# Performance work log

Hardware: AMD Instinct MI355X
Metric: run time of the kernel (lower is better)

The kernel has to match this reference:

```python
import jax, jax.numpy as jnp
import numpy as np

VOCAB, EMBED, MAXLEN, UNITS, F1, BATCH = 50000, 256, 512, 32, 16, 512

def setup_inputs() -> dict:
    key = jax.random.key(0)
    ks = jax.random.split(key, 9)
    tokens = jax.random.randint(ks[0], (BATCH, MAXLEN), 0, VOCAB, dtype=jnp.int32)
    emb_table = jax.random.normal(ks[1], (VOCAB, EMBED), dtype=jnp.float32) * 0.02
    # SimpleRNN params (Keras: kernel, recurrent_kernel, bias)
    Wx = jax.random.normal(ks[2], (EMBED, UNITS), dtype=jnp.float32) * (1.0 / np.sqrt(EMBED))
    Wh = jax.random.normal(ks[3], (UNITS, UNITS), dtype=jnp.float32) * (1.0 / np.sqrt(UNITS))
    b  = jnp.zeros((UNITS,), dtype=jnp.float32)
    W1 = jax.random.normal(ks[4], (UNITS, F1), dtype=jnp.float32) * (1.0 / np.sqrt(UNITS))
    b1 = jnp.zeros((F1,), dtype=jnp.float32)
    W2 = jax.random.normal(ks[5], (F1, 1), dtype=jnp.float32) * (1.0 / np.sqrt(F1))
    b2 = jnp.zeros((1,), dtype=jnp.float32)
    return {"tokens": tokens, "emb_table": emb_table, "Wx": Wx, "Wh": Wh, "b": b,
            "W1": W1, "b1": b1, "W2": W2, "b2": b2}

def reference(tokens, emb_table, Wx, Wh, b, W1, b1, W2, b2):
    # Embedding lookup: [B, T, E]
    x = emb_table[tokens]
    # SimpleRNN recurrence (tanh), return last hidden state. Dropout disabled (inference).
    xs = jnp.transpose(x, (1, 0, 2))  # time-major [T, B, E]
    h0 = jnp.zeros((tokens.shape[0], Wh.shape[0]), dtype=x.dtype)

    def step(h, x_t):
        h_new = jnp.tanh(x_t @ Wx + h @ Wh + b)
        return h_new, None

    h_last, _ = jax.lax.scan(step, h0, xs)
    # Flatten is a no-op on [B, 32]; Dense heads are linear (no activation), then sigmoid.
    z = (h_last @ W1 + b1) @ W2 + b2
    return jax.nn.sigmoid(z)  # [B, 1]
```

## Files before the change

kernel.cpp:

```cpp
#include <hip/hip_runtime.h>
#include <hip/hip_bf16.h>
#include <math.h>

#define TT 512
#define BB 512
#define EE 256
#define UU 32
#define FF1 16
#define NWAVE 2048

#define TWO_LOG2E 2.8853900817779268f

__device__ __forceinline__ float rdlane(float v, int lane) {
    return __int_as_float(__builtin_amdgcn_readlane(__float_as_int(v), lane));
}

#define DPP_ADD(v, ctrl)                                                    \
    (v) += __int_as_float(__builtin_amdgcn_update_dpp(                      \
        0, __float_as_int(v), (ctrl), 0xf, 0xf, true))

__global__ __launch_bounds__(64) void proj_dpp(
    const float* __restrict__ emb, const float* __restrict__ Wx,
    const float* __restrict__ bias, float* __restrict__ P, int nrows)
{
    const int L = threadIdx.x;
    const int g = L >> 4;
    const int c = L & 15;
    const int wv = blockIdx.x;

    float w[16][8];
    #pragma unroll
    for (int kk = 0; kk < 16; ++kk) {
        const float4* src = (const float4*)(Wx + (size_t)(kk * 16 + c) * UU + g * 8);
        float4 a = src[0], b = src[1];
        w[kk][0] = a.x; w[kk][1] = a.y; w[kk][2] = a.z; w[kk][3] = a.w;
        w[kk][4] = b.x; w[kk][5] = b.y; w[kk][6] = b.z; w[kk][7] = b.w;
    }
    float bs[8];
    #pragma unroll
    for (int uu = 0; uu < 8; ++uu) bs[uu] = bias[g * 8 + uu];

    auto rowptr = [&](int i) {
        int r = wv + NWAVE * i;
        if (r >= nrows) r = nrows - 1;
        return emb + (size_t)r * EE;
    };

    float xA[16], xB[16];
    {
        const float* rp = rowptr(0);
        #pragma unroll
        for (int kk = 0; kk < 16; ++kk) xA[kk] = rp[kk * 16 + c];
    }

    const int NI = (nrows - 1 - wv) / NWAVE + 1;

    for (int i = 0; i < NI; ++i) {
        {
            const float* rp = rowptr(i + 1 < NI ? i + 1 : i);
            #pragma unroll
            for (int kk = 0; kk < 16; ++kk) xB[kk] = rp[kk * 16 + c];
        }

        float p[8];
        #pragma unroll
        for (int uu = 0; uu < 8; ++uu) p[uu] = 0.f;
        #pragma unroll
        for (int kk = 0; kk < 16; ++kk) {
            const float xk = xA[kk];
            #pragma unroll
            for (int uu = 0; uu < 8; ++uu)
                p[uu] = fmaf(xk, w[kk][uu], p[uu]);
        }

        #pragma unroll
        for (int uu = 0; uu < 8; ++uu) {
            DPP_ADD(p[uu], 0x111);
            DPP_ADD(p[uu], 0x112);
            DPP_ADD(p[uu], 0x114);
            DPP_ADD(p[uu], 0x118);
        }

        if (c == 15) {
            const int r = wv + NWAVE * i;
            float4 o0, o1;
            o0.x = (p[0] + bs[0]) * TWO_LOG2E;
            o0.y = (p[1] + bs[1]) * TWO_LOG2E;
            o0.z = (p[2] + bs[2]) * TWO_LOG2E;
            o0.w = (p[3] + bs[3]) * TWO_LOG2E;
            o1.x = (p[4] + bs[4]) * TWO_LOG2E;
            o1.y = (p[5] + bs[5]) * TWO_LOG2E;
            o1.z = (p[6] + bs[6]) * TWO_LOG2E;
            o1.w = (p[7] + bs[7]) * TWO_LOG2E;
            float4* dst = (float4*)(P + (size_t)r * UU + g * 8);
            dst[0] = o0; dst[1] = o1;
        }

        #pragma unroll
        for (int kk = 0; kk < 16; ++kk) xA[kk] = xB[kk];
    }
}

__global__ __launch_bounds__(64) void scan_heads(
    const int* __restrict__ tokens, const float* __restrict__ P,
    const float* __restrict__ Wh,
    const float* __restrict__ W1, const float* __restrict__ b1,
    const float* __restrict__ W2, const float* __restrict__ b2,
    float* __restrict__ out)
{
    __shared__ float xs[TT * UU];

    const int L = threadIdx.x;
    const int u = L & 31;
    const int b = blockIdx.x;
    const int* trow = tokens + b * TT;

    float wh[UU];
    #pragma unroll
    for (int k = 0; k < UU; ++k) wh[k] = Wh[k * UU + u] * TWO_LOG2E;

    const int sub = L >> 3;
    const int q   = L & 7;
    for (int c = 0; c < 8; ++c) {
        int tk8[8];
        #pragma unroll
        for (int i = 0; i < 8; ++i)
            tk8[i] = trow[c * 64 + i * 8 + sub];
        #pragma unroll
        for (int i = 0; i < 8; ++i) {
            const float* src = P + (size_t)tk8[i] * UU + q * 4;
            float* dst = xs + (c * 64 + i * 8) * UU;
            __builtin_amdgcn_global_load_lds(
                (const __attribute__((address_space(1))) void*)src,
                (__attribute__((address_space(3))) void*)dst, 16, 0, 0);
        }
    }
    __syncthreads();

    float xr[8];
    #pragma unroll
    for (int j = 0; j < 8; ++j) xr[j] = xs[j * UU + u];

    float h = 0.f;

    for (int t = 0; t < TT; t += 8) {
        float xn[8];
        #pragma unroll
        for (int j = 0; j < 8; ++j)
            xn[j] = xs[((t + 8 + j) & (TT - 1)) * UU + u];

        #pragma unroll
        for (int j = 0; j < 8; ++j) {
            float hv[UU];
            #pragma unroll
            for (int k = 0; k < UU; ++k) hv[k] = rdlane(h, k);

            float a0 = fmaf(hv[0], wh[0], xr[j]);
            float a1 = hv[1] * wh[1];
            float a2 = hv[2] * wh[2];
            float a3 = hv[3] * wh[3];
            #pragma unroll
            for (int k = 4; k < UU; k += 4) {
                a0 = fmaf(hv[k],     wh[k],     a0);
                a1 = fmaf(hv[k + 1], wh[k + 1], a1);
                a2 = fmaf(hv[k + 2], wh[k + 2], a2);
                a3 = fmaf(hv[k + 3], wh[k + 3], a3);
            }
            float e = __builtin_amdgcn_exp2f((a0 + a1) + (a2 + a3));
            float r = __builtin_amdgcn_rcpf(e + 1.0f);
            h = fmaf(-2.0f, r, 1.0f);
        }

        #pragma unroll
        for (int j = 0; j < 8; ++j) xr[j] = xn[j];
    }

    const int j = threadIdx.x & 15;
    float s = b1[j];
    #pragma unroll
    for (int k = 0; k < UU; ++k) {
        float hk = rdlane(h, k);
        s = fmaf(hk, W1[k * FF1 + j], s);
    }
    float z = b2[0];
    #pragma unroll
    for (int jj = 0; jj < FF1; ++jj) {
        float yj = rdlane(s, jj);
        z = fmaf(yj, W2[jj], z);
    }
    if (threadIdx.x == 0) {
        float e = __builtin_amdgcn_exp2f(-z * 1.4426950408889634f);
        out[b] = __builtin_amdgcn_rcpf(1.0f + e);
    }
}

extern "C" void kernel_launch(void* const* d_in, const int* in_sizes, int n_in,
                              void* d_out, int out_size, void* d_ws, size_t ws_size,
                              hipStream_t stream) {
    const int*   tokens = (const int*)  d_in[0];
    const float* emb    = (const float*)d_in[1];
    const float* Wx     = (const float*)d_in[2];
    const float* Wh     = (const float*)d_in[3];
    const float* bias   = (const float*)d_in[4];
    const float* W1     = (const float*)d_in[5];
    const float* b1     = (const float*)d_in[6];
    const float* W2     = (const float*)d_in[7];
    const float* b2     = (const float*)d_in[8];
    float* out = (float*)d_out;

    const int vocab = in_sizes[1] / EE;
    float* P = (float*)d_ws;

    proj_dpp<<<dim3(NWAVE), dim3(64), 0, stream>>>(
        emb, Wx, bias, P, vocab);

    scan_heads<<<dim3(BB), dim3(64), 0, stream>>>(
        tokens, P, Wh, W1, b1, W2, b2, out);
}
```

Baseline: 182.7 us.

## Carry sigmoid-domain state in RNN scan and vectorize projection loads

The scan now carries r = 1/(1+e) as its state instead of h, folding h = 1 - 2r into the weights (wr = -2*wh) and into a per-unit constant S added to the inputs. This removes the final fma from the serial dependency chain of each step. Only the first 32 lanes run the scan, and the loop is double-buffered over 16 steps. Separately, the projection kernel loads embedding rows as float2 with a matching weight reorder, halving its load instructions; the algebraic refactor may change rounding slightly.

Measured after the change: 189.9 us. 3.9% more time.

```diff
diff --git a/kernel.cpp b/kernel.cpp
--- a/kernel.cpp
+++ b/kernel.cpp
@@ -28,49 +28,56 @@
     const int c = L & 15;
     const int wv = blockIdx.x;
 
-    float w[16][8];
+    float w[8][2][8];
     #pragma unroll
-    for (int kk = 0; kk < 16; ++kk) {
-        const float4* src = (const float4*)(Wx + (size_t)(kk * 16 + c) * UU + g * 8);
-        float4 a = src[0], b = src[1];
-        w[kk][0] = a.x; w[kk][1] = a.y; w[kk][2] = a.z; w[kk][3] = a.w;
-        w[kk][4] = b.x; w[kk][5] = b.y; w[kk][6] = b.z; w[kk][7] = b.w;
+    for (int kk = 0; kk < 8; ++kk) {
+        #pragma unroll
+        for (int d = 0; d < 2; ++d) {
+            const int row = 32 * kk + 2 * c + d;
+            const float4* src = (const float4*)(Wx + (size_t)row * UU + g * 8);
+            float4 a = src[0], b = src[1];
+            w[kk][d][0] = a.x; w[kk][d][1] = a.y; w[kk][d][2] = a.z; w[kk][d][3] = a.w;
+            w[kk][d][4] = b.x; w[kk][d][5] = b.y; w[kk][d][6] = b.z; w[kk][d][7] = b.w;
+        }
     }
     float bs[8];
     #pragma unroll
     for (int uu = 0; uu < 8; ++uu) bs[uu] = bias[g * 8 + uu];
 
-    auto rowptr = [&](int i) {
+    auto rowptr2 = [&](int i) {
         int r = wv + NWAVE * i;
         if (r >= nrows) r = nrows - 1;
-        return emb + (size_t)r * EE;
+        return (const float2*)(emb + (size_t)r * EE);
     };
 
-    float xA[16], xB[16];
+    float2 xA[8], xB[8];
     {
-        const float* rp = rowptr(0);
-        #pragma unroll
-        for (int kk = 0; kk < 16; ++kk) xA[kk] = rp[kk * 16 + c];
+        const float2* rp = rowptr2(0);
+        #pragma unroll
+        for (int kk = 0; kk < 8; ++kk) xA[kk] = rp[kk * 16 + c];
     }
 
     const int NI = (nrows - 1 - wv) / NWAVE + 1;
 
     for (int i = 0; i < NI; ++i) {
         {
-            const float* rp = rowptr(i + 1 < NI ? i + 1 : i);
-            #pragma unroll
-            for (int kk = 0; kk < 16; ++kk) xB[kk] = rp[kk * 16 + c];
+            const float2* rp = rowptr2(i + 1 < NI ? i + 1 : i);
+            #pragma unroll
+            for (int kk = 0; kk < 8; ++kk) xB[kk] = rp[kk * 16 + c];
         }
 
         float p[8];
         #pragma unroll
         for (int uu = 0; uu < 8; ++uu) p[uu] = 0.f;
         #pragma unroll
-        for (int kk = 0; kk < 16; ++kk) {
-            const float xk = xA[kk];
+        for (int kk = 0; kk < 8; ++kk) {
+            const float2 xp = xA[kk];
             #pragma unroll
             for (int uu = 0; uu < 8; ++uu)
-                p[uu] = fmaf(xk, w[kk][uu], p[uu]);
+                p[uu] = fmaf(xp.x, w[kk][0][uu], p[uu]);
+            #pragma unroll
+            for (int uu = 0; uu < 8; ++uu)
+                p[uu] = fmaf(xp.y, w[kk][1][uu], p[uu]);
         }
 
         #pragma unroll
@@ -97,7 +104,7 @@
         }
 
         #pragma unroll
-        for (int kk = 0; kk < 16; ++kk) xA[kk] = xB[kk];
+        for (int kk = 0; kk < 8; ++kk) xA[kk] = xB[kk];
     }
 }
 
@@ -115,9 +122,14 @@
     const int b = blockIdx.x;
     const int* trow = tokens + b * TT;
 
-    float wh[UU];
+    float wr[UU];
+    float S = 0.f;
     #pragma unroll
-    for (int k = 0; k < UU; ++k) wh[k] = Wh[k * UU + u] * TWO_LOG2E;
+    for (int k = 0; k < UU; ++k) {
+        float whk = Wh[k * UU + u] * TWO_LOG2E;
+        S += whk;
+        wr[k] = -2.0f * whk;
+    }
 
     const int sub = L >> 3;
     const int q   = L & 7;
@@ -137,60 +149,65 @@
     }
     __syncthreads();
 
-    float xr[8];
-    #pragma unroll
-    for (int j = 0; j < 8; ++j) xr[j] = xs[j * UU + u];
-
-    float h = 0.f;
-
-    for (int t = 0; t < TT; t += 8) {
-        float xn[8];
-        #pragma unroll
-        for (int j = 0; j < 8; ++j)
-            xn[j] = xs[((t + 8 + j) & (TT - 1)) * UU + u];
-
-        #pragma unroll
-        for (int j = 0; j < 8; ++j) {
-            float hv[UU];
-            #pragma unroll
-            for (int k = 0; k < UU; ++k) hv[k] = rdlane(h, k);
-
-            float a0 = fmaf(hv[0], wh[0], xr[j]);
-            float a1 = hv[1] * wh[1];
-            float a2 = hv[2] * wh[2];
-            float a3 = hv[3] * wh[3];
+    if (L < 32) {
+        float xA[8], xB[8];
+        #pragma unroll
+        for (int j = 0; j < 8; ++j) xA[j] = xs[j * UU + u] + S;
+
+        float r = 0.5f;
+
+        auto step = [&](float rc, float x) -> float {
+            float rv[UU];
+            #pragma unroll
+            for (int k = 0; k < UU; ++k) rv[k] = rdlane(rc, k);
+
+            float a0 = fmaf(rv[0], wr[0], x);
+            float a1 = rv[1] * wr[1];
+            float a2 = rv[2] * wr[2];
+            float a3 = rv[3] * wr[3];
             #pragma unroll
             for (int k = 4; k < UU; k += 4) {
-                a0 = fmaf(hv[k],     wh[k],     a0);
-                a1 = fmaf(hv[k + 1], wh[k + 1], a1);
-                a2 = fmaf(hv[k + 2], wh[k + 2], a2);
-                a3 = fmaf(hv[k + 3], wh[k + 3], a3);
+                a0 = fmaf(rv[k],     wr[k],     a0);
+                a1 = fmaf(rv[k + 1], wr[k + 1], a1);
+                a2 = fmaf(rv[k + 2], wr[k + 2], a2);
+                a3 = fmaf(rv[k + 3], wr[k + 3], a3);
             }
             float e = __builtin_amdgcn_exp2f((a0 + a1) + (a2 + a3));
-            float r = __builtin_amdgcn_rcpf(e + 1.0f);
-            h = fmaf(-2.0f, r, 1.0f);
-        }
-
-        #pragma unroll
-        for (int j = 0; j < 8; ++j) xr[j] = xn[j];
-    }
-
-    const int j = threadIdx.x & 15;
-    float s = b1[j];
-    #pragma unroll
-    for (int k = 0; k < UU; ++k) {
-        float hk = rdlane(h, k);
-        s = fmaf(hk, W1[k * FF1 + j], s);
-    }
-    float z = b2[0];
-    #pragma unroll
-    for (int jj = 0; jj < FF1; ++jj) {
-        float yj = rdlane(s, jj);
-        z = fmaf(yj, W2[jj], z);
-    }
-    if (threadIdx.x == 0) {
-        float e = __builtin_amdgcn_exp2f(-z * 1.4426950408889634f);
-        out[b] = __builtin_amdgcn_rcpf(1.0f + e);
+            return __builtin_amdgcn_rcpf(e + 1.0f);
+        };
+
+        for (int t = 0; t < TT; t += 16) {
+            #pragma unroll
+            for (int j = 0; j < 8; ++j)
+                xB[j] = xs[((t + 8 + j) & (TT - 1)) * UU + u] + S;
+            #pragma unroll
+            for (int j = 0; j < 8; ++j) r = step(r, xA[j]);
+            #pragma unroll
+            for (int j = 0; j < 8; ++j)
+                xA[j] = xs[((t + 16 + j) & (TT - 1)) * UU + u] + S;
+            #pragma unroll
+            for (int j = 0; j < 8; ++j) r = step(r, xB[j]);
+        }
+
+        float h = fmaf(-2.0f, r, 1.0f);
+
+        const int j = L & 15;
+        float s = b1[j];
+        #pragma unroll
+        for (int k = 0; k < UU; ++k) {
+            float hk = rdlane(h, k);
+            s = fmaf(hk, W1[k * FF1 + j], s);
+        }
+        float z = b2[0];
+        #pragma unroll
+        for (int jj = 0; jj < FF1; ++jj) {
+            float yj = rdlane(s, jj);
+            z = fmaf(yj, W2[jj], z);
+        }
+        if (L == 0) {
+            float e = __builtin_amdgcn_exp2f(-z * 1.4426950408889634f);
+            out[b] = __builtin_amdgcn_rcpf(1.0f + e);
+        }
     }
 }
 
```

## Replace readlane broadcast in RNN scan with DPP row-rotate and permlane32 swap

Applied to the files above, without the earlier changes.

The recurrent step no longer broadcasts the hidden state through 32 scalar readlanes. Each lane now gets the other units' values from the vector unit using DPP row-rotates within 16-lane rows plus a v_permlane32_swap to cross the 32-lane halves. Hidden units are remapped to lanes 0-15 and 32-47. The tanh is folded algebraically into the recurrence on r = 1/(1+e), with the weights prescaled by -2 and a constant S added, which saves one FMA per step. This removes the scalar readlane bottleneck on the serial dependency chain, at the cost of DPP hazard nops and a runtime probe of the rotate direction.

Result: slower. 193.9 us (+6.1%).

```diff
diff --git a/kernel.cpp b/kernel.cpp
--- a/kernel.cpp
+++ b/kernel.cpp
@@ -18,6 +18,10 @@
 #define DPP_ADD(v, ctrl)                                                    \
     (v) += __int_as_float(__builtin_amdgcn_update_dpp(                      \
         0, __float_as_int(v), (ctrl), 0xf, 0xf, true))
+
+#define RORF(dst, srcf, J)                                                  \
+    dst = __int_as_float(__builtin_amdgcn_update_dpp(                       \
+        0, __float_as_int(srcf), 0x120 | (J), 0xf, 0xf, true))
 
 __global__ __launch_bounds__(64) void proj_dpp(
     const float* __restrict__ emb, const float* __restrict__ Wx,
@@ -111,25 +115,36 @@
     __shared__ float xs[TT * UU];
 
     const int L = threadIdx.x;
-    const int u = L & 31;
+    const int c = L & 15;
+    const int u = c + ((L >> 5) << 4);
     const int b = blockIdx.x;
     const int* trow = tokens + b * TT;
 
-    float wh[UU];
-    #pragma unroll
-    for (int k = 0; k < UU; ++k) wh[k] = Wh[k * UU + u] * TWO_LOG2E;
+    int probe = __builtin_amdgcn_update_dpp(0, c, 0x121, 0xf, 0xf, true);
+    const int kstep = (__builtin_amdgcn_readfirstlane(probe) == 15) ? -1 : 1;
+
+    float wA[16], wB[16];
+    float S = 0.f;
+    #pragma unroll
+    for (int jj = 0; jj < 16; ++jj) {
+        const int kj = (c + kstep * jj) & 15;
+        wA[jj] = -2.0f * TWO_LOG2E * Wh[kj * UU + u];
+        wB[jj] = -2.0f * TWO_LOG2E * Wh[(16 + kj) * UU + u];
+    }
+    #pragma unroll
+    for (int k = 0; k < UU; ++k) S += TWO_LOG2E * Wh[k * UU + u];
 
     const int sub = L >> 3;
     const int q   = L & 7;
-    for (int c = 0; c < 8; ++c) {
+    for (int cc = 0; cc < 8; ++cc) {
         int tk8[8];
         #pragma unroll
         for (int i = 0; i < 8; ++i)
-            tk8[i] = trow[c * 64 + i * 8 + sub];
+            tk8[i] = trow[cc * 64 + i * 8 + sub];
         #pragma unroll
         for (int i = 0; i < 8; ++i) {
             const float* src = P + (size_t)tk8[i] * UU + q * 4;
-            float* dst = xs + (c * 64 + i * 8) * UU;
+            float* dst = xs + (cc * 64 + i * 8) * UU;
             __builtin_amdgcn_global_load_lds(
                 (const __attribute__((address_space(1))) void*)src,
                 (__attribute__((address_space(3))) void*)dst, 16, 0, 0);
@@ -139,48 +154,90 @@
 
     float xr[8];
     #pragma unroll
-    for (int j = 0; j < 8; ++j) xr[j] = xs[j * UU + u];
-
-    float h = 0.f;
+    for (int j = 0; j < 8; ++j) xr[j] = xs[j * UU + u] + S;
+
+    float r = 0.5f;
 
     for (int t = 0; t < TT; t += 8) {
         float xn[8];
         #pragma unroll
         for (int j = 0; j < 8; ++j)
-            xn[j] = xs[((t + 8 + j) & (TT - 1)) * UU + u];
+            xn[j] = xs[((t + 8 + j) & (TT - 1)) * UU + u] + S;
 
         #pragma unroll
         for (int j = 0; j < 8; ++j) {
-            float hv[UU];
-            #pragma unroll
-            for (int k = 0; k < UU; ++k) hv[k] = rdlane(h, k);
-
-            float a0 = fmaf(hv[0], wh[0], xr[j]);
-            float a1 = hv[1] * wh[1];
-            float a2 = hv[2] * wh[2];
-            float a3 = hv[3] * wh[3];
-            #pragma unroll
-            for (int k = 4; k < UU; k += 4) {
-                a0 = fmaf(hv[k],     wh[k],     a0);
-                a1 = fmaf(hv[k + 1], wh[k + 1], a1);
-                a2 = fmaf(hv[k + 2], wh[k + 2], a2);
-                a3 = fmaf(hv[k + 3], wh[k + 3], a3);
-            }
-            float e = __builtin_amdgcn_exp2f((a0 + a1) + (a2 + a3));
-            float r = __builtin_amdgcn_rcpf(e + 1.0f);
-            h = fmaf(-2.0f, r, 1.0f);
-        }
-
-        #pragma unroll
-        for (int j = 0; j < 8; ++j) xr[j] = xn[j];
-    }
-
-    const int j = threadIdx.x & 15;
-    float s = b1[j];
+            int aI = __float_as_int(r);
+            int bI = aI;
+            asm("s_nop 1\n\t"
+                "v_permlane32_swap_b32 %0, %1\n\t"
+                "s_nop 1"
+                : "+v"(aI), "+v"(bI));
+            float A  = __int_as_float(aI);
+            float Bv = __int_as_float(bI);
+
+            float va1, va2, va3, va4, va5, va6, va7, va8,
+                  va9, va10, va11, va12, va13, va14, va15;
+            float vb1, vb2, vb3, vb4, vb5, vb6, vb7, vb8,
+                  vb9, vb10, vb11, vb12, vb13, vb14, vb15;
+            RORF(va1,  A, 1);  RORF(va2,  A, 2);  RORF(va3,  A, 3);
+            RORF(va4,  A, 4);  RORF(va5,  A, 5);  RORF(va6,  A, 6);
+            RORF(va7,  A, 7);  RORF(va8,  A, 8);  RORF(va9,  A, 9);
+            RORF(va10, A, 10); RORF(va11, A, 11); RORF(va12, A, 12);
+            RORF(va13, A, 13); RORF(va14, A, 14); RORF(va15, A, 15);
+            RORF(vb1,  Bv, 1);  RORF(vb2,  Bv, 2);  RORF(vb3,  Bv, 3);
+            RORF(vb4,  Bv, 4);  RORF(vb5,  Bv, 5);  RORF(vb6,  Bv, 6);
+            RORF(vb7,  Bv, 7);  RORF(vb8,  Bv, 8);  RORF(vb9,  Bv, 9);
+            RORF(vb10, Bv, 10); RORF(vb11, Bv, 11); RORF(vb12, Bv, 12);
+            RORF(vb13, Bv, 13); RORF(vb14, Bv, 14); RORF(vb15, Bv, 15);
+
+            float p0 = fmaf(A,   wA[0], xr[j]);
+            float p1 = va1  * wA[1];
+            float p2 = va2  * wA[2];
+            float p3 = va3  * wA[3];
+            float p4 = va4  * wA[4];
+            float p5 = va5  * wA[5];
+            float p6 = va6  * wA[6];
+            float p7 = va7  * wA[7];
+            p0 = fmaf(va8,  wA[8],  p0);
+            p1 = fmaf(va9,  wA[9],  p1);
+            p2 = fmaf(va10, wA[10], p2);
+            p3 = fmaf(va11, wA[11], p3);
+            p4 = fmaf(va12, wA[12], p4);
+            p5 = fmaf(va13, wA[13], p5);
+            p6 = fmaf(va14, wA[14], p6);
+            p7 = fmaf(va15, wA[15], p7);
+            p0 = fmaf(Bv,   wB[0],  p0);
+            p1 = fmaf(vb1,  wB[1],  p1);
+            p2 = fmaf(vb2,  wB[2],  p2);
+            p3 = fmaf(vb3,  wB[3],  p3);
+            p4 = fmaf(vb4,  wB[4],  p4);
+            p5 = fmaf(vb5,  wB[5],  p5);
+            p6 = fmaf(vb6,  wB[6],  p6);
+            p7 = fmaf(vb7,  wB[7],  p7);
+            p0 = fmaf(vb8,  wB[8],  p0);
+            p1 = fmaf(vb9,  wB[9],  p1);
+            p2 = fmaf(vb10, wB[10], p2);
+            p3 = fmaf(vb11, wB[11], p3);
+            p4 = fmaf(vb12, wB[12], p4);
+            p5 = fmaf(vb13, wB[13], p5);
+            p6 = fmaf(vb14, wB[14], p6);
+            p7 = fmaf(vb15, wB[15], p7);
+
+            float s01 = p0 + p1, s23 = p2 + p3, s45 = p4 + p5, s67 = p6 + p7;
+            float e = __builtin_amdgcn_exp2f((s01 + s23) + (s45 + s67));
+            r = __builtin_amdgcn_rcpf(e + 1.0f);
+            xr[j] = xn[j];
+        }
+    }
+
+    float h = fmaf(-2.0f, r, 1.0f);
+
+    const int jh = L & 15;
+    float s = b1[jh];
     #pragma unroll
     for (int k = 0; k < UU; ++k) {
-        float hk = rdlane(h, k);
-        s = fmaf(hk, W1[k * FF1 + j], s);
+        float hk = rdlane(h, (k & 15) + ((k >> 4) << 5));
+        s = fmaf(hk, W1[k * FF1 + jh], s);
     }
     float z = b2[0];
     #pragma unroll
@@ -188,7 +245,7 @@
         float yj = rdlane(s, jj);
         z = fmaf(yj, W2[jj], z);
     }
-    if (threadIdx.x == 0) {
+    if (L == 0) {
         float e = __builtin_amdgcn_exp2f(-z * 1.4426950408889634f);
         out[b] = __builtin_amdgcn_rcpf(1.0f + e);
     }
```

## Carry sigmoid state in RNN scan and use packed FMA inline asm

Applied to the files above, without the earlier changes.

The recurrence now carries r = 1/(1+e) instead of h = 1-2r, folding the affine map into the recurrent weights (scaled by -2) and a per-unit constant added to the input projection. This removes one FMA from the serial dependency chain per step. The 32-term dot product is rewritten in inline assembly using readlane into SGPR pairs and v_pk_fma_f32, which halves the VALU instruction count. The asm hard-codes s40-s71 as clobbers and adds an s_nop, which limits what the compiler can schedule around it.

After: 187.7 us. 2.8% more time.

```diff
diff --git a/kernel.cpp b/kernel.cpp
--- a/kernel.cpp
+++ b/kernel.cpp
@@ -10,6 +10,8 @@
 #define NWAVE 2048
 
 #define TWO_LOG2E 2.8853900817779268f
+
+typedef float v2f __attribute__((ext_vector_type(2)));
 
 __device__ __forceinline__ float rdlane(float v, int lane) {
     return __int_as_float(__builtin_amdgcn_readlane(__float_as_int(v), lane));
@@ -115,21 +117,28 @@
     const int b = blockIdx.x;
     const int* trow = tokens + b * TT;
 
-    float wh[UU];
-    #pragma unroll
-    for (int k = 0; k < UU; ++k) wh[k] = Wh[k * UU + u] * TWO_LOG2E;
+    v2f w2[16];
+    float S = 0.f;
+    #pragma unroll
+    for (int p = 0; p < 16; ++p) {
+        float w0 = TWO_LOG2E * Wh[(2 * p) * UU + u];
+        float w1 = TWO_LOG2E * Wh[(2 * p + 1) * UU + u];
+        S += w0 + w1;
+        w2[p].x = -2.0f * w0;
+        w2[p].y = -2.0f * w1;
+    }
 
     const int sub = L >> 3;
     const int q   = L & 7;
-    for (int c = 0; c < 8; ++c) {
+    for (int cc = 0; cc < 8; ++cc) {
         int tk8[8];
         #pragma unroll
         for (int i = 0; i < 8; ++i)
-            tk8[i] = trow[c * 64 + i * 8 + sub];
+            tk8[i] = trow[cc * 64 + i * 8 + sub];
         #pragma unroll
         for (int i = 0; i < 8; ++i) {
             const float* src = P + (size_t)tk8[i] * UU + q * 4;
-            float* dst = xs + (c * 64 + i * 8) * UU;
+            float* dst = xs + (cc * 64 + i * 8) * UU;
             __builtin_amdgcn_global_load_lds(
                 (const __attribute__((address_space(1))) void*)src,
                 (__attribute__((address_space(3))) void*)dst, 16, 0, 0);
@@ -139,41 +148,90 @@
 
     float xr[8];
     #pragma unroll
-    for (int j = 0; j < 8; ++j) xr[j] = xs[j * UU + u];
-
-    float h = 0.f;
+    for (int j = 0; j < 8; ++j) xr[j] = xs[j * UU + u] + S;
+
+    float r = 0.5f;
 
     for (int t = 0; t < TT; t += 8) {
         float xn[8];
         #pragma unroll
         for (int j = 0; j < 8; ++j)
-            xn[j] = xs[((t + 8 + j) & (TT - 1)) * UU + u];
+            xn[j] = xs[((t + 8 + j) & (TT - 1)) * UU + u] + S;
 
         #pragma unroll
         for (int j = 0; j < 8; ++j) {
-            float hv[UU];
-            #pragma unroll
-            for (int k = 0; k < UU; ++k) hv[k] = rdlane(h, k);
-
-            float a0 = fmaf(hv[0], wh[0], xr[j]);
-            float a1 = hv[1] * wh[1];
-            float a2 = hv[2] * wh[2];
-            float a3 = hv[3] * wh[3];
-            #pragma unroll
-            for (int k = 4; k < UU; k += 4) {
-                a0 = fmaf(hv[k],     wh[k],     a0);
-                a1 = fmaf(hv[k + 1], wh[k + 1], a1);
-                a2 = fmaf(hv[k + 2], wh[k + 2], a2);
-                a3 = fmaf(hv[k + 3], wh[k + 3], a3);
-            }
-            float e = __builtin_amdgcn_exp2f((a0 + a1) + (a2 + a3));
-            float r = __builtin_amdgcn_rcpf(e + 1.0f);
-            h = fmaf(-2.0f, r, 1.0f);
-        }
-
-        #pragma unroll
-        for (int j = 0; j < 8; ++j) xr[j] = xn[j];
-    }
+            v2f a0, a1, a2, a3;
+            asm("s_nop 1\n\t"
+                "v_readlane_b32 s40, %4, 0\n\t"
+                "v_readlane_b32 s41, %4, 1\n\t"
+                "v_readlane_b32 s42, %4, 2\n\t"
+                "v_readlane_b32 s43, %4, 3\n\t"
+                "v_readlane_b32 s44, %4, 4\n\t"
+                "v_readlane_b32 s45, %4, 5\n\t"
+                "v_readlane_b32 s46, %4, 6\n\t"
+                "v_readlane_b32 s47, %4, 7\n\t"
+                "v_readlane_b32 s48, %4, 8\n\t"
+                "v_readlane_b32 s49, %4, 9\n\t"
+                "v_readlane_b32 s50, %4, 10\n\t"
+                "v_readlane_b32 s51, %4, 11\n\t"
+                "v_readlane_b32 s52, %4, 12\n\t"
+                "v_readlane_b32 s53, %4, 13\n\t"
+                "v_readlane_b32 s54, %4, 14\n\t"
+                "v_readlane_b32 s55, %4, 15\n\t"
+                "v_readlane_b32 s56, %4, 16\n\t"
+                "v_readlane_b32 s57, %4, 17\n\t"
+                "v_readlane_b32 s58, %4, 18\n\t"
+                "v_readlane_b32 s59, %4, 19\n\t"
+                "v_readlane_b32 s60, %4, 20\n\t"
+                "v_readlane_b32 s61, %4, 21\n\t"
+                "v_readlane_b32 s62, %4, 22\n\t"
+                "v_readlane_b32 s63, %4, 23\n\t"
+                "v_readlane_b32 s64, %4, 24\n\t"
+                "v_readlane_b32 s65, %4, 25\n\t"
+                "v_readlane_b32 s66, %4, 26\n\t"
+                "v_readlane_b32 s67, %4, 27\n\t"
+                "v_readlane_b32 s68, %4, 28\n\t"
+                "v_readlane_b32 s69, %4, 29\n\t"
+                "v_readlane_b32 s70, %4, 30\n\t"
+                "v_readlane_b32 s71, %4, 31\n\t"
+                "v_pk_mul_f32 %0, s[40:41], %5\n\t"
+                "v_pk_mul_f32 %1, s[42:43], %6\n\t"
+                "v_pk_mul_f32 %2, s[44:45], %7\n\t"
+                "v_pk_mul_f32 %3, s[46:47], %8\n\t"
+                "v_pk_fma_f32 %0, s[48:49], %9, %0\n\t"
+                "v_pk_fma_f32 %1, s[50:51], %10, %1\n\t"
+                "v_pk_fma_f32 %2, s[52:53], %11, %2\n\t"
+                "v_pk_fma_f32 %3, s[54:55], %12, %3\n\t"
+                "v_pk_fma_f32 %0, s[56:57], %13, %0\n\t"
+                "v_pk_fma_f32 %1, s[58:59], %14, %1\n\t"
+                "v_pk_fma_f32 %2, s[60:61], %15, %2\n\t"
+                "v_pk_fma_f32 %3, s[62:63], %16, %3\n\t"
+                "v_pk_fma_f32 %0, s[64:65], %17, %0\n\t"
+                "v_pk_fma_f32 %1, s[66:67], %18, %1\n\t"
+                "v_pk_fma_f32 %2, s[68:69], %19, %2\n\t"
+                "v_pk_fma_f32 %3, s[70:71], %20, %3"
+                : "=&v"(a0), "=&v"(a1), "=&v"(a2), "=&v"(a3)
+                : "v"(r),
+                  "v"(w2[0]),  "v"(w2[1]),  "v"(w2[2]),  "v"(w2[3]),
+                  "v"(w2[4]),  "v"(w2[5]),  "v"(w2[6]),  "v"(w2[7]),
+                  "v"(w2[8]),  "v"(w2[9]),  "v"(w2[10]), "v"(w2[11]),
+                  "v"(w2[12]), "v"(w2[13]), "v"(w2[14]), "v"(w2[15])
+                : "s40","s41","s42","s43","s44","s45","s46","s47",
+                  "s48","s49","s50","s51","s52","s53","s54","s55",
+                  "s56","s57","s58","s59","s60","s61","s62","s63",
+                  "s64","s65","s66","s67","s68","s69","s70","s71");
+
+            v2f t01 = a0 + a1;
+            v2f t23 = a2 + a3;
+            v2f tt  = t01 + t23;
+            float a = (tt.x + tt.y) + xr[j];
+            float e = __builtin_amdgcn_exp2f(a);
+            r = __builtin_amdgcn_rcpf(e + 1.0f);
+            xr[j] = xn[j];
+        }
+    }
+
+    float h = fmaf(-2.0f, r, 1.0f);
 
     const int j = threadIdx.x & 15;
     float s = b1[j];
```
